# Optimization experiments

Measured on AMD Instinct MI355X. Metric: run time of the kernel, lower is better.

The kernel has to match this reference:

```python
import jax, jax.numpy as jnp
import numpy as np

B, N, K, NUM_CLASSES = 8, 4096, 20, 40


def _knn_idx(x, k):
    # x: [B, N, D] -> indices of k nearest neighbors (self excluded), [B, N, k]
    sq = jnp.sum(x * x, axis=-1)  # [B, N]
    dist = sq[:, :, None] + sq[:, None, :] - 2.0 * jnp.einsum('bnd,bmd->bnm', x, x)
    dist = jnp.where(jnp.eye(x.shape[1], dtype=bool)[None], jnp.inf, dist)
    return jax.lax.top_k(-dist, k)[1]


def _edge_conv(x, idx, params):
    # PyG EdgeConv with max aggregation: max_j MLP([x_i, x_j - x_i])
    x_j = jax.vmap(lambda xb, ib: xb[ib])(x, idx)              # [B, N, K, D]
    x_i = jnp.broadcast_to(x[:, :, None, :], x_j.shape)        # [B, N, K, D]
    h = jnp.concatenate([x_i, x_j - x_i], axis=-1)             # [B, N, K, 2D]
    for w, b in params:
        h = jax.nn.relu(h @ w + b)
    return jnp.max(h, axis=2)                                  # [B, N, out]


def setup_inputs() -> dict:
    key = jax.random.key(0)
    ks = jax.random.split(key, 12)

    def lin(k, i, o):  # torch Linear default init
        k1, k2 = jax.random.split(k)
        s = 1.0 / np.sqrt(i)
        return (jax.random.uniform(k1, (i, o), jnp.float32, -s, s),
                jax.random.uniform(k2, (o,), jnp.float32, -s, s))

    inp = {
        'pos': jax.random.normal(ks[0], (B * N, 3), jnp.float32),
        'batch': jnp.repeat(jnp.arange(B, dtype=jnp.int32), N),
    }
    names = [('m1w1', 'm1b1', 6, 64), ('m1w2', 'm1b2', 64, 64), ('m1w3', 'm1b3', 64, 64),
             ('m2w1', 'm2b1', 128, 128), ('m2w2', 'm2b2', 128, 128), ('m2w3', 'm2b3', 128, 256),
             ('lin0_w', 'lin0_b', 256, 512), ('lin1_w', 'lin1_b', 512, 256),
             ('lin2_w', 'lin2_b', 256, 256), ('lin3_w', 'lin3_b', 256, NUM_CLASSES)]
    for t, (wn, bn, i, o) in enumerate(names):
        w, b = lin(ks[t + 1], i, o)
        inp[wn] = w
        inp[bn] = b
    return inp


def reference(pos, batch, m1w1, m1b1, m1w2, m1b2, m1w3, m1b3,
              m2w1, m2b1, m2w2, m2b2, m2w3, m2b3,
              lin0_w, lin0_b, lin1_w, lin1_b, lin2_w, lin2_b, lin3_w, lin3_b):
    x = pos.reshape(B, N, 3)
    x = _edge_conv(x, _knn_idx(x, K), [(m1w1, m1b1), (m1w2, m1b2), (m1w3, m1b3)])   # [B,N,64]
    x = _edge_conv(x, _knn_idx(x, K), [(m2w1, m2b1), (m2w2, m2b2), (m2w3, m2b3)])   # [B,N,256]
    x = jax.nn.relu(x @ lin0_w + lin0_b)                                            # [B,N,512]
    x = jax.ops.segment_max(x.reshape(B * N, -1), batch, num_segments=B)            # [B,512]
    x = jax.nn.relu(x @ lin1_w + lin1_b)
    x = jax.nn.relu(x @ lin2_w + lin2_b)   # dropout is identity in eval mode
    x = x @ lin3_w + lin3_b
    return jax.nn.log_softmax(x, axis=-1)
```

## Files before the change

### kernel.cpp

```cpp
#include <hip/hip_runtime.h>

#define DEVI static __device__ __forceinline__

typedef __attribute__((ext_vector_type(4))) float f32x4;
typedef __attribute__((ext_vector_type(8))) short short8;
typedef __attribute__((ext_vector_type(4))) short short4v;
typedef __attribute__((ext_vector_type(8))) __bf16 bf16x8;

#define N_    4096
#define KNN_  20
#define NPTS  32768

DEVI unsigned short f2bf(float f){
  unsigned u = __float_as_uint(f);
  u += 0x7FFFu + ((u >> 16) & 1u);
  return (unsigned short)(u >> 16);
}
DEVI float bf2f(unsigned short s){ return __uint_as_float(((unsigned)s) << 16); }
DEVI float bf2fs(short s){ return __uint_as_float(((unsigned)(unsigned short)s) << 16); }
DEVI unsigned umin32(unsigned a, unsigned b){ return a < b ? a : b; }
DEVI unsigned umax32(unsigned a, unsigned b){ return a > b ? a : b; }

DEVI f32x4 mfma16(short8 a, short8 b, f32x4 c){
  return __builtin_amdgcn_mfma_f32_16x16x32_bf16(
      __builtin_bit_cast(bf16x8, a), __builtin_bit_cast(bf16x8, b), c, 0, 0, 0);
}

DEVI short8 lds_frag(const unsigned short* buf, int row, int k0, int strideS, int swzMask){
  return *(const short8*)(buf + row*strideS + (k0 ^ ((row & swzMask) << 3)));
}
DEVI void lds_put8(unsigned short* buf, int row, int k0, int strideS, int swzMask, short8 v){
  *(short8*)(buf + row*strideS + (k0 ^ ((row & swzMask) << 3))) = v;
}
DEVI void lds_put1(unsigned short* buf, int row, int col, int strideS, int swzMask, unsigned short v){
  buf[row*strideS + (col ^ ((row & swzMask) << 3))] = v;
}

DEVI void ins32(unsigned K, unsigned (&a)[20]){
#pragma unroll
  for (int t = 19; t >= 1; --t) a[t] = umin32(a[t], umax32(a[t-1], K));
  a[0] = umin32(a[0], K);
}
DEVI void ins64(double K, double (&a)[20]){
#pragma unroll
  for (int t = 19; t >= 1; --t) a[t] = fmin(a[t], fmax(a[t-1], K));
  a[0] = fmin(a[0], K);
}

__global__ __launch_bounds__(256) void p3_k(const float* __restrict__ pos,
    unsigned short* __restrict__ p3h, unsigned short* __restrict__ p3l, float* __restrict__ nrm3){
  int p = blockIdx.x*256 + threadIdx.x;
  if (p >= NPTS) return;
  float x = pos[(size_t)p*3], y = pos[(size_t)p*3+1], z = pos[(size_t)p*3+2];
  float v[8] = {x, y, z, 0.f, 0.f, 0.f, 0.f, 0.f};
#pragma unroll
  for (int c = 0; c < 8; ++c){
    unsigned short h = f2bf(v[c]);
    p3h[(size_t)p*8 + c] = h;
    p3l[(size_t)p*8 + c] = f2bf(v[c] - bf2f(h));
  }
  nrm3[p] = fmaf(x, x, fmaf(y, y, z*z));
}

template<int MODE>
__global__ __launch_bounds__(256) void knn_k(const unsigned short* __restrict__ Xh,
                                             const unsigned short* __restrict__ Xl,
                                             const float* __restrict__ nrm,
                                             unsigned* __restrict__ pk){
  constexpr int OBL  = MODE ? 8192  : 1024;
  constexpr int OBUF = MODE ? 16384 : 2048;
  constexpr int OTHR = OBUF + 6144;
  constexpr int OSQ  = OTHR + 256;
  constexpr int SM   = MODE ? (OSQ + 256) : 15488;
  __shared__ __align__(16) char smem[SM];
  unsigned short* Bh = (unsigned short*)(smem);
  unsigned short* Bl = (unsigned short*)(smem + OBL);
  unsigned* buf      = (unsigned*)(smem + OBUF);
  unsigned* rowThr   = (unsigned*)(smem + OTHR);
  float* sqj         = (float*)(smem + OSQ);
  unsigned* mD       = (unsigned*)(smem);

  const int blk = blockIdx.x;
  const int rt = blk & 63, ch = (blk >> 6) & 1, bb = blk >> 7;
  const int rowbase = rt * 64, cbase = ch * 2048;
  const size_t gb = (size_t)bb * N_;
  const int tid = threadIdx.x, lane = tid & 63, wid = tid >> 6;
  const int l15 = lane & 15, g = lane >> 4, kL = g << 3, r0 = g << 2;
  const int qidx = wid*16 + l15;

  if (tid < 64) rowThr[tid] = 0xFFFFFFFFu;

  short8 qh0 = {0,0,0,0,0,0,0,0}, qh1 = {0,0,0,0,0,0,0,0};
  short8 ql0 = {0,0,0,0,0,0,0,0}, ql1 = {0,0,0,0,0,0,0,0};
  if (MODE == 1){
    const size_t ab = (gb + rowbase + qidx) * 64;
    qh0 = *(const short8*)(Xh + ab + kL);
    qh1 = *(const short8*)(Xh + ab + 32 + kL);
    ql0 = *(const short8*)(Xl + ab + kL);
    ql1 = *(const short8*)(Xl + ab + 32 + kL);
  } else {
    if (g == 0){
      const size_t ab = (gb + rowbase + qidx) * 8;
      qh0 = *(const short8*)(Xh + ab);
      ql0 = *(const short8*)(Xl + ab);
    }
  }
  const float si = nrm[gb + rowbase + qidx];

  unsigned arr[20];
#pragma unroll
  for (int t = 0; t < 20; ++t) arr[t] = 0xFFFFFFFFu;
  int cnt = 0;
  bool selfR[4];
#pragma unroll
  for (int r = 0; r < 4; ++r) selfR[r] = (l15 == r0 + r);

  if (MODE == 1){
    for (int f = tid; f < 512; f += 256){
      int lf = f & 63, half = (f >> 6) & 1, ct = f >> 7;
      int row = ct*16 + (lf & 15);
      int col = half*32 + ((lf >> 4) << 3);
      const size_t src = (gb + cbase + row) * 64 + col;
      *(short8*)(Bh + f*8) = *(const short8*)(Xh + src);
      *(short8*)(Bl + f*8) = *(const short8*)(Xl + src);
    }
  } else {
    if (tid < 64)       *(short8*)(Bh + tid*8)      = *(const short8*)(Xh + (gb + cbase + tid)*8);
    else if (tid < 128) *(short8*)(Bl + (tid-64)*8) = *(const short8*)(Xl + (gb + cbase + (tid-64))*8);
  }
  if (tid < 64) sqj[tid] = nrm[gb + cbase + tid];
  __syncthreads();

  for (int c = 0; c < 32; ++c){
    const bool selfTile = (cbase + c*64 == rowbase);
    unsigned kb16[16];
#pragma unroll
    for (int ct = 0; ct < 4; ++ct){
      f32x4 acc = {0.f,0.f,0.f,0.f};
      if (MODE == 1){
        const int fb = lane*8;
        short8 ch0 = *(const short8*)(Bh + (ct*2+0)*512 + fb);
        short8 ch1 = *(const short8*)(Bh + (ct*2+1)*512 + fb);
        short8 cl0 = *(const short8*)(Bl + (ct*2+0)*512 + fb);
        short8 cl1 = *(const short8*)(Bl + (ct*2+1)*512 + fb);
        acc = mfma16(ch0, qh0, acc); acc = mfma16(ch1, qh1, acc);
        acc = mfma16(cl0, qh0, acc); acc = mfma16(cl1, qh1, acc);
        acc = mfma16(ch0, ql0, acc); acc = mfma16(ch1, ql1, acc);
      } else {
        short8 cb = {0,0,0,0,0,0,0,0}, cl_ = {0,0,0,0,0,0,0,0};
        if (g == 0){
          cb  = *(const short8*)(Bh + (ct*16 + l15)*8);
          cl_ = *(const short8*)(Bl + (ct*16 + l15)*8);
        }
        acc = mfma16(cb,  qh0, acc);
        acc = mfma16(cl_, qh0, acc);
        acc = mfma16(cb,  ql0, acc);
      }
      f32x4 sj4 = *(const f32x4*)(sqj + ct*16 + r0);
#pragma unroll
      for (int r = 0; r < 4; ++r){
        unsigned cid = (unsigned)(c*64 + ct*16 + r0 + r);
        float dv = fmaxf(fmaf(-2.f, acc[r], si + sj4[r]), 0.f);
        unsigned kb = (__float_as_uint(dv) & ~0x7FFu) | cid;
        if (selfTile && ct == wid && selfR[r]) kb = 0x7F800000u | cid;
        kb16[ct*4 + r] = kb;
      }
    }
    short8 nh0 = {0,0,0,0,0,0,0,0}, nh1 = {0,0,0,0,0,0,0,0};
    short8 nl0 = {0,0,0,0,0,0,0,0}, nl1 = {0,0,0,0,0,0,0,0};
    float nsq = 0.f;
    const bool more = (c + 1 < 32);
    if (more){
      if (MODE == 1){
#pragma unroll
        for (int ff = 0; ff < 2; ++ff){
          int f = tid + ff*256;
          int lf = f & 63, half = (f >> 6) & 1, ct = f >> 7;
          int row = ct*16 + (lf & 15);
          int col = half*32 + ((lf >> 4) << 3);
          const size_t src = (gb + cbase + (c+1)*64 + row) * 64 + col;
          if (ff == 0){ nh0 = *(const short8*)(Xh + src); nl0 = *(const short8*)(Xl + src); }
          else        { nh1 = *(const short8*)(Xh + src); nl1 = *(const short8*)(Xl + src); }
        }
      } else {
        if (tid < 64)       nh0 = *(const short8*)(Xh + (gb + cbase + (c+1)*64 + tid)*8);
        else if (tid < 128) nl0 = *(const short8*)(Xl + (gb + cbase + (c+1)*64 + (tid-64))*8);
      }
      if (tid < 64) nsq = nrm[gb + cbase + (c+1)*64 + tid];
    }
    {
      unsigned thrP = rowThr[qidx];
#pragma unroll
      for (int i = 0; i < 16; ++i){
        unsigned kb = kb16[i];
        if (kb < thrP){
          if (cnt < 6){ buf[cnt*256 + tid] = kb; ++cnt; }
          else ins32(kb, arr);
        }
      }
      for (int t = 0; t < cnt; ++t) ins32(buf[t*256 + tid], arr);
      cnt = 0;
      atomicMin(&rowThr[qidx], arr[19]);
    }
    __syncthreads();
    if (more){
      if (MODE == 1){
        *(short8*)(Bh + tid*8)       = nh0;
        *(short8*)(Bh + (tid+256)*8) = nh1;
        *(short8*)(Bl + tid*8)       = nl0;
        *(short8*)(Bl + (tid+256)*8) = nl1;
      } else {
        if (tid < 64)       *(short8*)(Bh + tid*8)      = nh0;
        else if (tid < 128) *(short8*)(Bl + (tid-64)*8) = nl0;
      }
      if (tid < 64) sqj[tid] = nsq;
    }
    __syncthreads();
  }
  __syncthreads();
  if (g > 0){
#pragma unroll
    for (int t = 0; t < 20; ++t) mD[(qidx*3 + g-1)*20 + t] = arr[t];
  }
  __syncthreads();
  if (g == 0){
    for (int gg = 0; gg < 3; ++gg)
#pragma unroll
      for (int t = 0; t < 20; ++t) ins32(mD[(qidx*3 + gg)*20 + t], arr);
    const size_t gp = gb + rowbase + qidx;
#pragma unroll
    for (int t = 0; t < 20; ++t) pk[((size_t)(ch*20 + t))*NPTS + gp] = arr[t];
  }
}

__global__ __launch_bounds__(256) void knn_merge_k(const unsigned* __restrict__ pk,
                                                   int* __restrict__ idx){
  const int p = blockIdx.x*256 + threadIdx.x;
  double arr[20];
#pragma unroll
  for (int t = 0; t < 20; ++t){
    unsigned k = pk[(size_t)t*NPTS + p];
    unsigned long long K = (((unsigned long long)(k & ~0x7FFu)) << 1) | (k & 0x7FFu);
    arr[t] = __builtin_bit_cast(double, K);
  }
#pragma unroll
  for (int t = 0; t < 20; ++t){
    unsigned k = pk[(size_t)(20 + t)*NPTS + p];
    unsigned long long K = (((unsigned long long)(k & ~0x7FFu)) << 1) | (2048u + (k & 0x7FFu));
    ins64(__builtin_bit_cast(double, K), arr);
  }
  int* o = idx + (size_t)p*KNN_;
#pragma unroll
  for (int t = 0; t < 20; ++t)
    o[t] = (int)(__builtin_bit_cast(unsigned long long, arr[t]) & 0xFFFu);
}

__global__ void stage_w_k(const float* __restrict__ src, unsigned short* __restrict__ dh,
                          unsigned short* __restrict__ dl, int K, int Nw, int KT, int NT){
  int tid = blockIdx.x*256 + threadIdx.x;
  if (tid >= NT*KT*64) return;
  int l = tid & 63;
  int kk = (tid >> 6) % KT;
  int nt = tid / (64*KT);
  int n = nt*16 + (l & 15);
  int kb = kk*32 + ((l >> 4) << 3);
#pragma unroll
  for (int e=0;e<8;++e){
    int k = kb + e;
    float w = (k < K) ? src[(size_t)k*Nw + n] : 0.f;
    unsigned short h = f2bf(w);
    dh[(size_t)tid*8 + e] = h;
    if (dl) dl[(size_t)tid*8 + e] = f2bf(w - bf2f(h));
  }
}

__global__ __launch_bounds__(256) void ec1_k(const float* __restrict__ pos, const int* __restrict__ idx1,
    const unsigned short* __restrict__ W1h, const unsigned short* __restrict__ W1l,
    const unsigned short* __restrict__ W2h, const unsigned short* __restrict__ W2l,
    const unsigned short* __restrict__ W3h, const unsigned short* __restrict__ W3l,
    const float* __restrict__ b1, const float* __restrict__ b2, const float* __restrict__ b3,
    unsigned short* __restrict__ x1h, unsigned short* __restrict__ x1l, float* __restrict__ nrm1){
  __shared__ __align__(16) char smem[52224];
  unsigned short* Ah  = (unsigned short*)(smem);
  unsigned short* Al  = (unsigned short*)(smem + 5120);
  unsigned short* H1h = (unsigned short*)(smem + 10240);
  unsigned short* H1l = (unsigned short*)(smem + 20480);
  unsigned short* H2h = (unsigned short*)(smem + 30720);
  unsigned short* H2l = (unsigned short*)(smem + 40960);
  unsigned* pmax = (unsigned*)(smem + 51200);
  const int p0 = blockIdx.x * 4;
  const int bb = p0 >> 12;
  const int tid = threadIdx.x, lane = tid & 63, wid = tid >> 6;
  pmax[tid] = 0u;
  if (tid < 80){
    int p = p0 + tid/20, slot = tid%20;
    int j = idx1[(size_t)p*KNN_ + slot];
    int gj = (bb << 12) + j;
    float a6[6];
    a6[0] = pos[(size_t)p*3]; a6[1] = pos[(size_t)p*3+1]; a6[2] = pos[(size_t)p*3+2];
    a6[3] = pos[(size_t)gj*3]   - a6[0];
    a6[4] = pos[(size_t)gj*3+1] - a6[1];
    a6[5] = pos[(size_t)gj*3+2] - a6[2];
#pragma unroll
    for (int q=0;q<4;++q){
      short8 vh, vl;
#pragma unroll
      for (int c=0;c<8;++c){
        int cc = q*8+c;
        float v = 0.f;
        if (cc < 6) v = a6[cc];
        unsigned short h = f2bf(v);
        vh[c] = (short)h;
        vl[c] = (short)f2bf(v - bf2f(h));
      }
      lds_put8(Ah, tid, q*8, 32, 3, vh);
      lds_put8(Al, tid, q*8, 32, 3, vl);
    }
  }
  __syncthreads();
  const int l15 = lane & 15, kL = (lane >> 4) << 3, r0 = (lane >> 4) << 2;
  {
    int nt = wid;
    short8 wh = *(const short8*)(W1h + ((size_t)nt*64 + lane)*8);
    short8 wl = *(const short8*)(W1l + ((size_t)nt*64 + lane)*8);
    float bias = b1[nt*16 + l15];
    for (int mt=0; mt<5; ++mt){
      int ar = mt*16 + l15;
      short8 ah = lds_frag(Ah, ar, kL, 32, 3);
      short8 al = lds_frag(Al, ar, kL, 32, 3);
      f32x4 acc = {0.f,0.f,0.f,0.f};
      acc = mfma16(ah, wh, acc);
      acc = mfma16(ah, wl, acc);
      acc = mfma16(al, wh, acc);
#pragma unroll
      for (int r=0;r<4;++r){
        int row = mt*16 + r0 + r;
        float v = fmaxf(acc[r] + bias, 0.f);
        unsigned short h = f2bf(v);
        lds_put1(H1h, row, nt*16+l15, 64, 7, h);
        lds_put1(H1l, row, nt*16+l15, 64, 7, f2bf(v - bf2f(h)));
      }
    }
  }
  __syncthreads();
  {
    int nt = wid;
    short8 wh0 = *(const short8*)(W2h + ((size_t)(nt*2+0)*64 + lane)*8);
    short8 wh1 = *(const short8*)(W2h + ((size_t)(nt*2+1)*64 + lane)*8);
    short8 wl0 = *(const short8*)(W2l + ((size_t)(nt*2+0)*64 + lane)*8);
    short8 wl1 = *(const short8*)(W2l + ((size_t)(nt*2+1)*64 + lane)*8);
    float bias = b2[nt*16 + l15];
    for (int mt=0; mt<5; ++mt){
      int ar = mt*16 + l15;
      short8 ah0 = lds_frag(H1h, ar, kL,      64, 7);
      short8 ah1 = lds_frag(H1h, ar, 32 + kL, 64, 7);
      short8 al0 = lds_frag(H1l, ar, kL,      64, 7);
      short8 al1 = lds_frag(H1l, ar, 32 + kL, 64, 7);
      f32x4 acc = {0.f,0.f,0.f,0.f};
      acc = mfma16(ah0, wh0, acc); acc = mfma16(ah1, wh1, acc);
      acc = mfma16(ah0, wl0, acc); acc = mfma16(ah1, wl1, acc);
      acc = mfma16(al0, wh0, acc); acc = mfma16(al1, wh1, acc);
#pragma unroll
      for (int r=0;r<4;++r){
        int row = mt*16 + r0 + r;
        float v = fmaxf(acc[r] + bias, 0.f);
        unsigned short h = f2bf(v);
        lds_put1(H2h, row, nt*16+l15, 64, 7, h);
        lds_put1(H2l, row, nt*16+l15, 64, 7, f2bf(v - bf2f(h)));
      }
    }
  }
  __syncthreads();
  {
    int nt = wid;
    short8 wh0 = *(const short8*)(W3h + ((size_t)(nt*2+0)*64 + lane)*8);
    short8 wh1 = *(const short8*)(W3h + ((size_t)(nt*2+1)*64 + lane)*8);
    short8 wl0 = *(const short8*)(W3l + ((size_t)(nt*2+0)*64 + lane)*8);
    short8 wl1 = *(const short8*)(W3l + ((size_t)(nt*2+1)*64 + lane)*8);
    float bias = b3[nt*16 + l15];
    for (int mt=0; mt<5; ++mt){
      int ar = mt*16 + l15;
      short8 ah0 = lds_frag(H2h, ar, kL,      64, 7);
      short8 ah1 = lds_frag(H2h, ar, 32 + kL, 64, 7);
      short8 al0 = lds_frag(H2l, ar, kL,      64, 7);
      short8 al1 = lds_frag(H2l, ar, 32 + kL, 64, 7);
      f32x4 acc = {0.f,0.f,0.f,0.f};
      acc = mfma16(ah0, wh0, acc); acc = mfma16(ah1, wh1, acc);
      acc = mfma16(ah0, wl0, acc); acc = mfma16(ah1, wl1, acc);
      acc = mfma16(al0, wh0, acc); acc = mfma16(al1, wh1, acc);
#pragma unroll
      for (int r=0;r<4;++r){
        int row = mt*16 + r0 + r;
        float v = fmaxf(acc[r] + bias, 0.f);
        atomicMax(&pmax[(row/20)*64 + nt*16 + l15], __float_as_uint(v));
      }
    }
  }
  __syncthreads();
  if (tid < 128){
    int p = tid >> 5, cp = tid & 31;
    int c0 = cp*2, c1 = c0 + 1;
    float m0 = __uint_as_float(pmax[p*64 + c0]);
    float m1 = __uint_as_float(pmax[p*64 + c1]);
    int gp = p0 + p;
    unsigned short h0 = f2bf(m0), h1v = f2bf(m1);
    x1h[(size_t)gp*64 + c0] = h0;
    x1h[(size_t)gp*64 + c1] = h1v;
    x1l[(size_t)gp*64 + c0] = f2bf(m0 - bf2f(h0));
    x1l[(size_t)gp*64 + c1] = f2bf(m1 - bf2f(h1v));
    float s = fmaf(m0, m0, m1*m1);
    s += __shfl_xor(s, 1, 32); s += __shfl_xor(s, 2, 32); s += __shfl_xor(s, 4, 32);
    s += __shfl_xor(s, 8, 32); s += __shfl_xor(s, 16, 32);
    if (cp == 0) nrm1[gp] = s;
  }
}

__global__ __launch_bounds__(256) void ec2_k(const unsigned short* __restrict__ x1h, const int* __restrict__ idx2,
    const unsigned short* __restrict__ V1, const unsigned short* __restrict__ V2, const unsigned short* __restrict__ V3,
    const float* __restrict__ b1, const float* __restrict__ b2, const float* __restrict__ b3,
    unsigned short* __restrict__ x2b){
  __shared__ __align__(16) char smem[81920];
  unsigned short* A  = (unsigned short*)(smem);
  unsigned short* H1 = (unsigned short*)(smem + 40960);
  const int p0 = blockIdx.x * 8, bb = p0 >> 12;
  const int tid = threadIdx.x, lane = tid & 63, wid = tid >> 6;
  const int l15 = lane & 15, r0 = (lane >> 4) << 2;

  if (tid < 160){
    int p = p0 + tid/20, slot = tid%20;
    int j = idx2[(size_t)p*KNN_ + slot];
    int gj = (bb << 12) + j;
    const unsigned short* xi = x1h + (size_t)p*64;
    const unsigned short* xj = x1h + (size_t)gj*64;
    int mt = tid >> 4, lrow = tid & 15;
#pragma unroll
    for (int q=0;q<8;++q){
      short8 vi = *(const short8*)(xi + q*8);
      short8 vj = *(const short8*)(xj + q*8);
      short8 vd;
#pragma unroll
      for (int c=0;c<8;++c) vd[c] = (short)f2bf(bf2fs(vj[c]) - bf2fs(vi[c]));
      *(short8*)(A + (((mt*4 + (q>>2))*64) + (q&3)*16 + lrow)*8) = vi;
      *(short8*)(A + (((mt*4 + 2 + (q>>2))*64) + (q&3)*16 + lrow)*8) = vd;
    }
  }
  __syncthreads();

  {
    short8 w[2][4];
#pragma unroll
    for (int ni=0;ni<2;++ni)
#pragma unroll
      for (int kk=0;kk<4;++kk)
        w[ni][kk] = *(const short8*)(V1 + ((size_t)((wid*2+ni)*4+kk)*64 + lane)*8);
    f32x4 b4[2];
    b4[0] = *(const f32x4*)(b1 + (wid*2+0)*16 + r0);
    b4[1] = *(const f32x4*)(b1 + (wid*2+1)*16 + r0);
    for (int mt=0; mt<10; ++mt){
      short8 bfr[4];
#pragma unroll
      for (int kk=0;kk<4;++kk) bfr[kk] = *(const short8*)(A + ((mt*4+kk)*64 + lane)*8);
#pragma unroll
      for (int ni=0;ni<2;++ni){
        int nt = wid*2 + ni;
        f32x4 acc = {0.f,0.f,0.f,0.f};
#pragma unroll
        for (int kk=0;kk<4;++kk) acc = mfma16(w[ni][kk], bfr[kk], acc);
        short4v v4;
#pragma unroll
        for (int r=0;r<4;++r) v4[r] = (short)f2bf(fmaxf(acc[r] + b4[ni][r], 0.f));
        int kk2 = nt >> 1, sub2 = (nt & 1)*2 + (r0 >> 3);
        *(short4v*)(H1 + ((mt*4+kk2)*64 + sub2*16 + l15)*8 + (r0 & 4)) = v4;
      }
    }
  }
  __syncthreads();
  {
    short8 w[2][4];
#pragma unroll
    for (int ni=0;ni<2;++ni)
#pragma unroll
      for (int kk=0;kk<4;++kk)
        w[ni][kk] = *(const short8*)(V2 + ((size_t)((wid*2+ni)*4+kk)*64 + lane)*8);
    f32x4 b4[2];
    b4[0] = *(const f32x4*)(b2 + (wid*2+0)*16 + r0);
    b4[1] = *(const f32x4*)(b2 + (wid*2+1)*16 + r0);
    for (int mt=0; mt<10; ++mt){
      short8 bfr[4];
#pragma unroll
      for (int kk=0;kk<4;++kk) bfr[kk] = *(const short8*)(H1 + ((mt*4+kk)*64 + lane)*8);
#pragma unroll
      for (int ni=0;ni<2;++ni){
        int nt = wid*2 + ni;
        f32x4 acc = {0.f,0.f,0.f,0.f};
#pragma unroll
        for (int kk=0;kk<4;++kk) acc = mfma16(w[ni][kk], bfr[kk], acc);
        short4v v4;
#pragma unroll
        for (int r=0;r<4;++r) v4[r] = (short)f2bf(fmaxf(acc[r] + b4[ni][r], 0.f));
        int kk2 = nt >> 1, sub2 = (nt & 1)*2 + (r0 >> 3);
        *(short4v*)(A + ((mt*4+kk2)*64 + sub2*16 + l15)*8 + (r0 & 4)) = v4;
      }
    }
  }
  __syncthreads();
  for (int g2=0; g2<2; ++g2){
    {
      short8 w[2][4];
#pragma unroll
      for (int ni=0;ni<2;++ni)
#pragma unroll
        for (int kk=0;kk<4;++kk)
          w[ni][kk] = *(const short8*)(V3 + ((size_t)((g2*8 + wid*2+ni)*4+kk)*64 + lane)*8);
      f32x4 b4[2];
      b4[0] = *(const f32x4*)(b3 + (g2*8 + wid*2+0)*16 + r0);
      b4[1] = *(const f32x4*)(b3 + (g2*8 + wid*2+1)*16 + r0);
      for (int mt=0; mt<10; ++mt){
        short8 bfr[4];
#pragma unroll
        for (int kk=0;kk<4;++kk) bfr[kk] = *(const short8*)(A + ((mt*4+kk)*64 + lane)*8);
#pragma unroll
        for (int ni=0;ni<2;++ni){
          int ntl = wid*2 + ni;
          f32x4 acc = {0.f,0.f,0.f,0.f};
#pragma unroll
          for (int kk=0;kk<4;++kk) acc = mfma16(w[ni][kk], bfr[kk], acc);
          short4v v4;
#pragma unroll
          for (int r=0;r<4;++r) v4[r] = (short)f2bf(fmaxf(acc[r] + b4[ni][r], 0.f));
          int kk2 = ntl >> 1, sub2 = (ntl & 1)*2 + (r0 >> 3);
          *(short4v*)(H1 + ((mt*4+kk2)*64 + sub2*16 + l15)*8 + (r0 & 4)) = v4;
        }
      }
    }
    __syncthreads();
    if (tid < 128){
      int p = tid >> 4, c8 = tid & 15;
      int kk = c8 >> 2, sub = c8 & 3;
      unsigned short mx[8];
#pragma unroll
      for (int e=0;e<8;++e) mx[e] = 0;
      for (int e=0;e<20;++e){
        int ee = e + p + c8; ee -= (ee >= 20) ? 20 : 0; ee -= (ee >= 20) ? 20 : 0;
        int row = p*20 + ee;
        short8 v = *(const short8*)(H1 + (((row>>4)*4 + kk)*64 + sub*16 + (row & 15))*8);
#pragma unroll
        for (int k2=0;k2<8;++k2){
          unsigned short u = (unsigned short)v[k2];
          mx[k2] = u > mx[k2] ? u : mx[k2];
        }
      }
      short8 o;
#pragma unroll
      for (int k2=0;k2<8;++k2) o[k2] = (short)mx[k2];
      *(short8*)(x2b + (size_t)(p0 + p)*256 + g2*128 + c8*8) = o;
    }
    __syncthreads();
  }
}

__global__ __launch_bounds__(256) void lin0_k(const unsigned short* __restrict__ x2b, const unsigned short* __restrict__ W0s,
                                              const float* __restrict__ b0, unsigned* __restrict__ pool){
  __shared__ __align__(16) char smem[67584];
  unsigned short* A = (unsigned short*)(smem);
  unsigned* ploc = (unsigned*)(smem + 65536);
  const int blk = blockIdx.x; const size_t row0 = (size_t)blk * 128; const int bb = blk >> 5;
  const int tid = threadIdx.x, lane = tid & 63, wid = tid >> 6;
  for (int it = tid; it < 4096; it += 256){
    int row = it >> 5, q = (it & 31) << 3;
    lds_put8(A, row, q, 256, 7, *(const short8*)(x2b + (row0 + row)*256 + q));
  }
  ploc[tid] = 0u; ploc[tid+256] = 0u;
  __syncthreads();
  const int l15 = lane & 15, kL = (lane >> 4) << 3;
  short8 af[2][8];
#pragma unroll
  for (int m=0;m<2;++m)
#pragma unroll
    for (int kk=0;kk<8;++kk)
      af[m][kk] = lds_frag(A, (wid*2+m)*16 + l15, kk*32 + kL, 256, 7);
  for (int nt=0; nt<32; ++nt){
    f32x4 a0 = {0.f,0.f,0.f,0.f}, a1 = {0.f,0.f,0.f,0.f};
#pragma unroll
    for (int kk=0;kk<8;++kk){
      short8 w = *(const short8*)(W0s + ((size_t)(nt*8+kk)*64 + lane)*8);
      a0 = mfma16(af[0][kk], w, a0);
      a1 = mfma16(af[1][kk], w, a1);
    }
    int col = nt*16 + l15;
    float m = fmaxf(fmaxf(fmaxf(a0[0],a0[1]),fmaxf(a0[2],a0[3])),
                    fmaxf(fmaxf(a1[0],a1[1]),fmaxf(a1[2],a1[3])));
    m = fmaxf(m + b0[col], 0.f);
    atomicMax(&ploc[col], __float_as_uint(m));
  }
  __syncthreads();
  atomicMax(&pool[(size_t)bb*512 + tid], ploc[tid]);
  atomicMax(&pool[(size_t)bb*512 + tid + 256], ploc[tid+256]);
}

__global__ __launch_bounds__(256) void head_k(const unsigned* __restrict__ pool,
    const float* __restrict__ w1, const float* __restrict__ bb1,
    const float* __restrict__ w2, const float* __restrict__ bb2,
    const float* __restrict__ w3, const float* __restrict__ bb3,
    float* __restrict__ out){
  __shared__ float pl[8*512];
  __shared__ float y1[8*256];
  __shared__ float y2[8*256];
  __shared__ float lg[8*40];
  const int tid = threadIdx.x;
  for (int it = tid; it < 4096; it += 256) pl[it] = __uint_as_float(pool[it]);
  __syncthreads();
  {
    float acc[8]; float bv = bb1[tid];
#pragma unroll
    for (int r=0;r<8;++r) acc[r] = bv;
    for (int k=0;k<512;++k){
      float w = w1[(size_t)k*256 + tid];
#pragma unroll
      for (int r=0;r<8;++r) acc[r] = fmaf(pl[r*512+k], w, acc[r]);
    }
#pragma unroll
    for (int r=0;r<8;++r) y1[r*256+tid] = fmaxf(acc[r], 0.f);
  }
  __syncthreads();
  {
    float acc[8]; float bv = bb2[tid];
#pragma unroll
    for (int r=0;r<8;++r) acc[r] = bv;
    for (int k=0;k<256;++k){
      float w = w2[(size_t)k*256 + tid];
#pragma unroll
      for (int r=0;r<8;++r) acc[r] = fmaf(y1[r*256+k], w, acc[r]);
    }
#pragma unroll
    for (int r=0;r<8;++r) y2[r*256+tid] = fmaxf(acc[r], 0.f);
  }
  __syncthreads();
  if (tid < 40){
    float acc[8]; float bv = bb3[tid];
#pragma unroll
    for (int r=0;r<8;++r) acc[r] = bv;
    for (int k=0;k<256;++k){
      float w = w3[(size_t)k*40 + tid];
#pragma unroll
      for (int r=0;r<8;++r) acc[r] = fmaf(y2[r*256+k], w, acc[r]);
    }
#pragma unroll
    for (int r=0;r<8;++r) lg[r*40+tid] = acc[r];
  }
  __syncthreads();
  if (tid < 8){
    float m = -__builtin_inff();
    for (int c2=0;c2<40;++c2) m = fmaxf(m, lg[tid*40+c2]);
    float s = 0.f;
    for (int c2=0;c2<40;++c2) s += expf(lg[tid*40+c2] - m);
    float L = logf(s);
    for (int c2=0;c2<40;++c2) out[tid*40+c2] = lg[tid*40+c2] - m - L;
  }
}

extern "C" void kernel_launch(void* const* d_in, const int* in_sizes, int n_in,
                              void* d_out, int out_size, void* d_ws, size_t ws_size,
                              hipStream_t stream){
  (void)in_sizes; (void)n_in; (void)out_size; (void)ws_size;
  const float* pos  = (const float*)d_in[0];
  const float* m1w1 = (const float*)d_in[2];  const float* m1b1 = (const float*)d_in[3];
  const float* m1w2 = (const float*)d_in[4];  const float* m1b2 = (const float*)d_in[5];
  const float* m1w3 = (const float*)d_in[6];  const float* m1b3 = (const float*)d_in[7];
  const float* m2w1 = (const float*)d_in[8];  const float* m2b1 = (const float*)d_in[9];
  const float* m2w2 = (const float*)d_in[10]; const float* m2b2 = (const float*)d_in[11];
  const float* m2w3 = (const float*)d_in[12]; const float* m2b3 = (const float*)d_in[13];
  const float* l0w  = (const float*)d_in[14]; const float* l0b  = (const float*)d_in[15];
  const float* l1w  = (const float*)d_in[16]; const float* l1b  = (const float*)d_in[17];
  const float* l2w  = (const float*)d_in[18]; const float* l2b  = (const float*)d_in[19];
  const float* l3w  = (const float*)d_in[20]; const float* l3b  = (const float*)d_in[21];

  char* ws = (char*)d_ws;
  size_t o = 0;
  auto alloc = [&](size_t bytes){ size_t r = o; o += (bytes + 255) & ~(size_t)255; return r; };
  size_t o_idx1 = alloc((size_t)NPTS*20*4);
  size_t o_idx2 = alloc((size_t)NPTS*20*4);
  size_t o_x1h  = alloc((size_t)NPTS*64*2);
  size_t o_x1l  = alloc((size_t)NPTS*64*2);
  size_t o_nrm  = alloc((size_t)NPTS*4);
  size_t o_x2b  = alloc((size_t)NPTS*256*2);
  size_t o_pool = alloc(8*512*4);
  size_t o_p3h  = alloc((size_t)NPTS*8*2);
  size_t o_p3l  = alloc((size_t)NPTS*8*2);
  size_t o_nrm3 = alloc((size_t)NPTS*4);
  size_t o_pk   = alloc((size_t)2*20*NPTS*4);
  size_t o_W1h = alloc(4*1*64*8*2),  o_W1l = alloc(4*1*64*8*2);
  size_t o_W2h = alloc(4*2*64*8*2),  o_W2l = alloc(4*2*64*8*2);
  size_t o_W3h = alloc(4*2*64*8*2),  o_W3l = alloc(4*2*64*8*2);
  size_t o_V1  = alloc(8*4*64*8*2);
  size_t o_V2  = alloc(8*4*64*8*2);
  size_t o_V3  = alloc(16*4*64*8*2);
  size_t o_W0  = alloc(32*8*64*8*2);

  hipMemsetAsync(ws + o_pool, 0, 8*512*4, stream);

  stage_w_k<<<1,256,0,stream>>>(m1w1, (unsigned short*)(ws+o_W1h), (unsigned short*)(ws+o_W1l), 6, 64, 1, 4);
  stage_w_k<<<2,256,0,stream>>>(m1w2, (unsigned short*)(ws+o_W2h), (unsigned short*)(ws+o_W2l), 64, 64, 2, 4);
  stage_w_k<<<2,256,0,stream>>>(m1w3, (unsigned short*)(ws+o_W3h), (unsigned short*)(ws+o_W3l), 64, 64, 2, 4);
  stage_w_k<<<8,256,0,stream>>>(m2w1, (unsigned short*)(ws+o_V1), nullptr, 128, 128, 4, 8);
  stage_w_k<<<8,256,0,stream>>>(m2w2, (unsigned short*)(ws+o_V2), nullptr, 128, 128, 4, 8);
  stage_w_k<<<16,256,0,stream>>>(m2w3, (unsigned short*)(ws+o_V3), nullptr, 128, 256, 4, 16);
  stage_w_k<<<64,256,0,stream>>>(l0w,  (unsigned short*)(ws+o_W0), nullptr, 256, 512, 8, 32);

  p3_k<<<128,256,0,stream>>>(pos, (unsigned short*)(ws+o_p3h), (unsigned short*)(ws+o_p3l), (float*)(ws+o_nrm3));

  knn_k<0><<<1024,256,0,stream>>>((const unsigned short*)(ws+o_p3h), (const unsigned short*)(ws+o_p3l),
                                  (const float*)(ws+o_nrm3), (unsigned*)(ws+o_pk));
  knn_merge_k<<<128,256,0,stream>>>((const unsigned*)(ws+o_pk), (int*)(ws+o_idx1));

  ec1_k<<<8192,256,0,stream>>>(pos, (const int*)(ws+o_idx1),
      (const unsigned short*)(ws+o_W1h), (const unsigned short*)(ws+o_W1l),
      (const unsigned short*)(ws+o_W2h), (const unsigned short*)(ws+o_W2l),
      (const unsigned short*)(ws+o_W3h), (const unsigned short*)(ws+o_W3l),
      m1b1, m1b2, m1b3,
      (unsigned short*)(ws+o_x1h), (unsigned short*)(ws+o_x1l), (float*)(ws+o_nrm));

  knn_k<1><<<1024,256,0,stream>>>((const unsigned short*)(ws+o_x1h), (const unsigned short*)(ws+o_x1l),
                                  (const float*)(ws+o_nrm), (unsigned*)(ws+o_pk));
  knn_merge_k<<<128,256,0,stream>>>((const unsigned*)(ws+o_pk), (int*)(ws+o_idx2));

  ec2_k<<<4096,256,0,stream>>>((const unsigned short*)(ws+o_x1h), (const int*)(ws+o_idx2),
      (const unsigned short*)(ws+o_V1), (const unsigned short*)(ws+o_V2), (const unsigned short*)(ws+o_V3),
      m2b1, m2b2, m2b3, (unsigned short*)(ws+o_x2b));

  lin0_k<<<256,256,0,stream>>>((const unsigned short*)(ws+o_x2b), (const unsigned short*)(ws+o_W0),
                               l0b, (unsigned*)(ws+o_pool));

  head_k<<<1,256,0,stream>>>((const unsigned*)(ws+o_pool), l1w, l1b, l2w, l2b, l3w, l3b, (float*)d_out);
}
```

Baseline: 656.1 us.

## Double-buffer kNN column tiles and restructure EdgeConv1 MLP LDS layout

The kNN kernel now keeps two LDS buffers for the candidate column tile. The next tile's global loads are issued before the MFMA and top-k work, which removes one barrier per iteration and hides load latency. The first EdgeConv kernel swaps the MFMA operand order so each lane writes four contiguous outputs straight into fragment-ordered LDS, replacing scattered scalar swizzled stores. It also replaces the per-element LDS atomicMax with a dump-then-reduce pass. The cost is doubled LDS use in kNN, which may lower occupancy, plus an extra reduction pass in EdgeConv.

```diff
diff --git a/kernel.cpp b/kernel.cpp
--- a/kernel.cpp
+++ b/kernel.cpp
@@ -31,9 +31,6 @@
 }
 DEVI void lds_put8(unsigned short* buf, int row, int k0, int strideS, int swzMask, short8 v){
   *(short8*)(buf + row*strideS + (k0 ^ ((row & swzMask) << 3))) = v;
-}
-DEVI void lds_put1(unsigned short* buf, int row, int col, int strideS, int swzMask, unsigned short v){
-  buf[row*strideS + (col ^ ((row & swzMask) << 3))] = v;
 }
 
 DEVI void ins32(unsigned K, unsigned (&a)[20]){
@@ -67,17 +64,18 @@
                                              const unsigned short* __restrict__ Xl,
                                              const float* __restrict__ nrm,
                                              unsigned* __restrict__ pk){
-  constexpr int OBL  = MODE ? 8192  : 1024;
-  constexpr int OBUF = MODE ? 16384 : 2048;
+  constexpr int BSTR = MODE ? 4096 : 512;
+  constexpr int OBL  = MODE ? 16384 : 2048;
+  constexpr int OBUF = MODE ? 32768 : 4096;
   constexpr int OTHR = OBUF + 6144;
   constexpr int OSQ  = OTHR + 256;
-  constexpr int SM   = MODE ? (OSQ + 256) : 15488;
+  constexpr int SM   = MODE ? (OSQ + 512) : 15360;
   __shared__ __align__(16) char smem[SM];
-  unsigned short* Bh = (unsigned short*)(smem);
-  unsigned short* Bl = (unsigned short*)(smem + OBL);
+  unsigned short* BhA = (unsigned short*)(smem);
+  unsigned short* BlA = (unsigned short*)(smem + OBL);
   unsigned* buf      = (unsigned*)(smem + OBUF);
   unsigned* rowThr   = (unsigned*)(smem + OTHR);
-  float* sqj         = (float*)(smem + OSQ);
+  float* sqjA        = (float*)(smem + OSQ);
   unsigned* mD       = (unsigned*)(smem);
 
   const int blk = blockIdx.x;
@@ -121,18 +119,46 @@
       int row = ct*16 + (lf & 15);
       int col = half*32 + ((lf >> 4) << 3);
       const size_t src = (gb + cbase + row) * 64 + col;
-      *(short8*)(Bh + f*8) = *(const short8*)(Xh + src);
-      *(short8*)(Bl + f*8) = *(const short8*)(Xl + src);
+      *(short8*)(BhA + f*8) = *(const short8*)(Xh + src);
+      *(short8*)(BlA + f*8) = *(const short8*)(Xl + src);
     }
   } else {
-    if (tid < 64)       *(short8*)(Bh + tid*8)      = *(const short8*)(Xh + (gb + cbase + tid)*8);
-    else if (tid < 128) *(short8*)(Bl + (tid-64)*8) = *(const short8*)(Xl + (gb + cbase + (tid-64))*8);
-  }
-  if (tid < 64) sqj[tid] = nrm[gb + cbase + tid];
+    if (tid < 64)       *(short8*)(BhA + tid*8)      = *(const short8*)(Xh + (gb + cbase + tid)*8);
+    else if (tid < 128) *(short8*)(BlA + (tid-64)*8) = *(const short8*)(Xl + (gb + cbase + (tid-64))*8);
+  }
+  if (tid < 64) sqjA[tid] = nrm[gb + cbase + tid];
   __syncthreads();
 
   for (int c = 0; c < 32; ++c){
+    const int cur = c & 1;
+    const unsigned short* Bh = BhA + cur*BSTR;
+    const unsigned short* Bl = BlA + cur*BSTR;
+    const float* sqj = sqjA + cur*64;
     const bool selfTile = (cbase + c*64 == rowbase);
+    const bool more = (c + 1 < 32);
+
+    short8 nh0 = {0,0,0,0,0,0,0,0}, nh1 = {0,0,0,0,0,0,0,0};
+    short8 nl0 = {0,0,0,0,0,0,0,0}, nl1 = {0,0,0,0,0,0,0,0};
+    float nsq = 0.f;
+    if (more){
+      if (MODE == 1){
+#pragma unroll
+        for (int ff = 0; ff < 2; ++ff){
+          int f = tid + ff*256;
+          int lf = f & 63, half = (f >> 6) & 1, ct = f >> 7;
+          int row = ct*16 + (lf & 15);
+          int col = half*32 + ((lf >> 4) << 3);
+          const size_t src = (gb + cbase + (c+1)*64 + row) * 64 + col;
+          if (ff == 0){ nh0 = *(const short8*)(Xh + src); nl0 = *(const short8*)(Xl + src); }
+          else        { nh1 = *(const short8*)(Xh + src); nl1 = *(const short8*)(Xl + src); }
+        }
+      } else {
+        if (tid < 64)       nh0 = *(const short8*)(Xh + (gb + cbase + (c+1)*64 + tid)*8);
+        else if (tid < 128) nl0 = *(const short8*)(Xl + (gb + cbase + (c+1)*64 + (tid-64))*8);
+      }
+      if (tid < 64) nsq = nrm[gb + cbase + (c+1)*64 + tid];
+    }
+
     unsigned kb16[16];
 #pragma unroll
     for (int ct = 0; ct < 4; ++ct){
@@ -166,28 +192,7 @@
         kb16[ct*4 + r] = kb;
       }
     }
-    short8 nh0 = {0,0,0,0,0,0,0,0}, nh1 = {0,0,0,0,0,0,0,0};
-    short8 nl0 = {0,0,0,0,0,0,0,0}, nl1 = {0,0,0,0,0,0,0,0};
-    float nsq = 0.f;
-    const bool more = (c + 1 < 32);
-    if (more){
-      if (MODE == 1){
-#pragma unroll
-        for (int ff = 0; ff < 2; ++ff){
-          int f = tid + ff*256;
-          int lf = f & 63, half = (f >> 6) & 1, ct = f >> 7;
-          int row = ct*16 + (lf & 15);
-          int col = half*32 + ((lf >> 4) << 3);
-          const size_t src = (gb + cbase + (c+1)*64 + row) * 64 + col;
-          if (ff == 0){ nh0 = *(const short8*)(Xh + src); nl0 = *(const short8*)(Xl + src); }
-          else        { nh1 = *(const short8*)(Xh + src); nl1 = *(const short8*)(Xl + src); }
-        }
-      } else {
-        if (tid < 64)       nh0 = *(const short8*)(Xh + (gb + cbase + (c+1)*64 + tid)*8);
-        else if (tid < 128) nl0 = *(const short8*)(Xl + (gb + cbase + (c+1)*64 + (tid-64))*8);
-      }
-      if (tid < 64) nsq = nrm[gb + cbase + (c+1)*64 + tid];
-    }
+
     {
       unsigned thrP = rowThr[qidx];
 #pragma unroll
@@ -202,18 +207,20 @@
       cnt = 0;
       atomicMin(&rowThr[qidx], arr[19]);
     }
-    __syncthreads();
+
     if (more){
+      unsigned short* BhN = BhA + (cur^1)*BSTR;
+      unsigned short* BlN = BlA + (cur^1)*BSTR;
       if (MODE == 1){
-        *(short8*)(Bh + tid*8)       = nh0;
-        *(short8*)(Bh + (tid+256)*8) = nh1;
-        *(short8*)(Bl + tid*8)       = nl0;
-        *(short8*)(Bl + (tid+256)*8) = nl1;
+        *(short8*)(BhN + tid*8)       = nh0;
+        *(short8*)(BhN + (tid+256)*8) = nh1;
+        *(short8*)(BlN + tid*8)       = nl0;
+        *(short8*)(BlN + (tid+256)*8) = nl1;
       } else {
-        if (tid < 64)       *(short8*)(Bh + tid*8)      = nh0;
-        else if (tid < 128) *(short8*)(Bl + (tid-64)*8) = nl0;
-      }
-      if (tid < 64) sqj[tid] = nsq;
+        if (tid < 64)       *(short8*)(BhN + tid*8)      = nh0;
+        else if (tid < 128) *(short8*)(BlN + (tid-64)*8) = nl0;
+      }
+      if (tid < 64) sqjA[(cur^1)*64 + tid] = nsq;
     }
     __syncthreads();
   }
@@ -280,18 +287,19 @@
     const unsigned short* __restrict__ W3h, const unsigned short* __restrict__ W3l,
     const float* __restrict__ b1, const float* __restrict__ b2, const float* __restrict__ b3,
     unsigned short* __restrict__ x1h, unsigned short* __restrict__ x1l, float* __restrict__ nrm1){
-  __shared__ __align__(16) char smem[52224];
+  __shared__ __align__(16) char smem[51200];
   unsigned short* Ah  = (unsigned short*)(smem);
   unsigned short* Al  = (unsigned short*)(smem + 5120);
   unsigned short* H1h = (unsigned short*)(smem + 10240);
   unsigned short* H1l = (unsigned short*)(smem + 20480);
   unsigned short* H2h = (unsigned short*)(smem + 30720);
   unsigned short* H2l = (unsigned short*)(smem + 40960);
-  unsigned* pmax = (unsigned*)(smem + 51200);
+  float* dump = (float*)(smem);
   const int p0 = blockIdx.x * 4;
   const int bb = p0 >> 12;
   const int tid = threadIdx.x, lane = tid & 63, wid = tid >> 6;
-  pmax[tid] = 0u;
+  const int l15 = lane & 15, g = lane >> 4, r0 = g << 2;
+
   if (tid < 80){
     int p = p0 + tid/20, slot = tid%20;
     int j = idx1[(size_t)p*KNN_ + slot];
@@ -301,117 +309,126 @@
     a6[3] = pos[(size_t)gj*3]   - a6[0];
     a6[4] = pos[(size_t)gj*3+1] - a6[1];
     a6[5] = pos[(size_t)gj*3+2] - a6[2];
-#pragma unroll
-    for (int q=0;q<4;++q){
-      short8 vh, vl;
-#pragma unroll
-      for (int c=0;c<8;++c){
-        int cc = q*8+c;
-        float v = 0.f;
-        if (cc < 6) v = a6[cc];
-        unsigned short h = f2bf(v);
-        vh[c] = (short)h;
-        vl[c] = (short)f2bf(v - bf2f(h));
-      }
-      lds_put8(Ah, tid, q*8, 32, 3, vh);
-      lds_put8(Al, tid, q*8, 32, 3, vl);
-    }
-  }
-  __syncthreads();
-  const int l15 = lane & 15, kL = (lane >> 4) << 3, r0 = (lane >> 4) << 2;
+    int mt = tid >> 4, lrow = tid & 15;
+    short8 vh, vl, zz = {0,0,0,0,0,0,0,0};
+#pragma unroll
+    for (int c=0;c<8;++c){
+      float v = (c < 6) ? a6[c] : 0.f;
+      unsigned short h = f2bf(v);
+      vh[c] = (short)h;
+      vl[c] = (short)f2bf(v - bf2f(h));
+    }
+    *(short8*)(Ah + (mt*64 + lrow)*8) = vh;
+    *(short8*)(Al + (mt*64 + lrow)*8) = vl;
+#pragma unroll
+    for (int gg=1;gg<4;++gg){
+      *(short8*)(Ah + (mt*64 + gg*16 + lrow)*8) = zz;
+      *(short8*)(Al + (mt*64 + gg*16 + lrow)*8) = zz;
+    }
+  }
+  __syncthreads();
+  const int nt = wid;
+  const int kk2 = nt >> 1, sub2 = (nt & 1)*2 + (g >> 1), e0 = (g & 1)*4;
   {
-    int nt = wid;
     short8 wh = *(const short8*)(W1h + ((size_t)nt*64 + lane)*8);
     short8 wl = *(const short8*)(W1l + ((size_t)nt*64 + lane)*8);
-    float bias = b1[nt*16 + l15];
+    f32x4 b4 = *(const f32x4*)(b1 + nt*16 + r0);
     for (int mt=0; mt<5; ++mt){
-      int ar = mt*16 + l15;
-      short8 ah = lds_frag(Ah, ar, kL, 32, 3);
-      short8 al = lds_frag(Al, ar, kL, 32, 3);
+      short8 ah = *(const short8*)(Ah + (mt*64 + lane)*8);
+      short8 al = *(const short8*)(Al + (mt*64 + lane)*8);
       f32x4 acc = {0.f,0.f,0.f,0.f};
-      acc = mfma16(ah, wh, acc);
-      acc = mfma16(ah, wl, acc);
-      acc = mfma16(al, wh, acc);
+      acc = mfma16(wh, ah, acc);
+      acc = mfma16(wl, ah, acc);
+      acc = mfma16(wh, al, acc);
+      short4v vh4, vl4;
 #pragma unroll
       for (int r=0;r<4;++r){
-        int row = mt*16 + r0 + r;
-        float v = fmaxf(acc[r] + bias, 0.f);
+        float v = fmaxf(acc[r] + b4[r], 0.f);
         unsigned short h = f2bf(v);
-        lds_put1(H1h, row, nt*16+l15, 64, 7, h);
-        lds_put1(H1l, row, nt*16+l15, 64, 7, f2bf(v - bf2f(h)));
-      }
+        vh4[r] = (short)h;
+        vl4[r] = (short)f2bf(v - bf2f(h));
+      }
+      *(short4v*)(H1h + ((mt*2 + kk2)*64 + sub2*16 + l15)*8 + e0) = vh4;
+      *(short4v*)(H1l + ((mt*2 + kk2)*64 + sub2*16 + l15)*8 + e0) = vl4;
     }
   }
   __syncthreads();
   {
-    int nt = wid;
     short8 wh0 = *(const short8*)(W2h + ((size_t)(nt*2+0)*64 + lane)*8);
     short8 wh1 = *(const short8*)(W2h + ((size_t)(nt*2+1)*64 + lane)*8);
     short8 wl0 = *(const short8*)(W2l + ((size_t)(nt*2+0)*64 + lane)*8);
     short8 wl1 = *(const short8*)(W2l + ((size_t)(nt*2+1)*64 + lane)*8);
-    float bias = b2[nt*16 + l15];
+    f32x4 b4 = *(const f32x4*)(b2 + nt*16 + r0);
     for (int mt=0; mt<5; ++mt){
-      int ar = mt*16 + l15;
-      short8 ah0 = lds_frag(H1h, ar, kL,      64, 7);
-      short8 ah1 = lds_frag(H1h, ar, 32 + kL, 64, 7);
-      short8 al0 = lds_frag(H1l, ar, kL,      64, 7);
-      short8 al1 = lds_frag(H1l, ar, 32 + kL, 64, 7);
+      short8 ah0 = *(const short8*)(H1h + ((mt*2+0)*64 + lane)*8);
+      short8 ah1 = *(const short8*)(H1h + ((mt*2+1)*64 + lane)*8);
+      short8 al0 = *(const short8*)(H1l + ((mt*2+0)*64 + lane)*8);
+      short8 al1 = *(const short8*)(H1l + ((mt*2+1)*64 + lane)*8);
       f32x4 acc = {0.f,0.f,0.f,0.f};
-      acc = mfma16(ah0, wh0, acc); acc = mfma16(ah1, wh1, acc);
-      acc = mfma16(ah0, wl0, acc); acc = mfma16(ah1, wl1, acc);
-      acc = mfma16(al0, wh0, acc); acc = mfma16(al1, wh1, acc);
+      acc = mfma16(wh0, ah0, acc); acc = mfma16(wh1, ah1, acc);
+      acc = mfma16(wl0, ah0, acc); acc = mfma16(wl1, ah1, acc);
+      acc = mfma16(wh0, al0, acc); acc = mfma16(wh1, al1, acc);
+      short4v vh4, vl4;
 #pragma unroll
       for (int r=0;r<4;++r){
-        int row = mt*16 + r0 + r;
-        float v = fmaxf(acc[r] + bias, 0.f);
+        float v = fmaxf(acc[r] + b4[r], 0.f);
         unsigned short h = f2bf(v);
-        lds_put1(H2h, row, nt*16+l15, 64, 7, h);
-        lds_put1(H2l, row, nt*16+l15, 64, 7, f2bf(v - bf2f(h)));
-      }
+        vh4[r] = (short)h;
+        vl4[r] = (short)f2bf(v - bf2f(h));
+      }
+      *(short4v*)(H2h + ((mt*2 + kk2)*64 + sub2*16 + l15)*8 + e0) = vh4;
+      *(short4v*)(H2l + ((mt*2 + kk2)*64 + sub2*16 + l15)*8 + e0) = vl4;
     }
   }
   __syncthreads();
   {
-    int nt = wid;
     short8 wh0 = *(const short8*)(W3h + ((size_t)(nt*2+0)*64 + lane)*8);
     short8 wh1 = *(const short8*)(W3h + ((size_t)(nt*2+1)*64 + lane)*8);
     short8 wl0 = *(const short8*)(W3l + ((size_t)(nt*2+0)*64 + lane)*8);
     short8 wl1 = *(const short8*)(W3l + ((size_t)(nt*2+1)*64 + lane)*8);
-    float bias = b3[nt*16 + l15];
+    f32x4 b4 = *(const f32x4*)(b3 + nt*16 + r0);
     for (int mt=0; mt<5; ++mt){
-      int ar = mt*16 + l15;
-      short8 ah0 = lds_frag(H2h, ar, kL,      64, 7);
-      short8 ah1 = lds_frag(H2h, ar, 32 + kL, 64, 7);
-      short8 al0 = lds_frag(H2l, ar, kL,      64, 7);
-      short8 al1 = lds_frag(H2l, ar, 32 + kL, 64, 7);
+      short8 ah0 = *(const short8*)(H2h + ((mt*2+0)*64 + lane)*8);
+      short8 ah1 = *(const short8*)(H2h + ((mt*2+1)*64 + lane)*8);
+      short8 al0 = *(const short8*)(H2l + ((mt*2+0)*64 + lane)*8);
+      short8 al1 = *(const short8*)(H2l + ((mt*2+1)*64 + lane)*8);
       f32x4 acc = {0.f,0.f,0.f,0.f};
-      acc = mfma16(ah0, wh0, acc); acc = mfma16(ah1, wh1, acc);
-      acc = mfma16(ah0, wl0, acc); acc = mfma16(ah1, wl1, acc);
-      acc = mfma16(al0, wh0, acc); acc = mfma16(al1, wh1, acc);
-#pragma unroll
-      for (int r=0;r<4;++r){
-        int row = mt*16 + r0 + r;
-        float v = fmaxf(acc[r] + bias, 0.f);
-        atomicMax(&pmax[(row/20)*64 + nt*16 + l15], __float_as_uint(v));
-      }
-    }
-  }
-  __syncthreads();
-  if (tid < 128){
-    int p = tid >> 5, cp = tid & 31;
-    int c0 = cp*2, c1 = c0 + 1;
-    float m0 = __uint_as_float(pmax[p*64 + c0]);
-    float m1 = __uint_as_float(pmax[p*64 + c1]);
+      acc = mfma16(wh0, ah0, acc); acc = mfma16(wh1, ah1, acc);
+      acc = mfma16(wl0, ah0, acc); acc = mfma16(wl1, ah1, acc);
+      acc = mfma16(wh0, al0, acc); acc = mfma16(wh1, al1, acc);
+      f32x4 o;
+#pragma unroll
+      for (int r=0;r<4;++r) o[r] = fmaxf(acc[r] + b4[r], 0.f);
+      int edge = mt*16 + l15;
+      *(f32x4*)(dump + edge*68 + nt*16 + r0) = o;
+    }
+  }
+  __syncthreads();
+  if (tid < 64){
+    int p = tid >> 4, c4 = tid & 15;
+    int st = tid % 20;
+    float mx[4] = {0.f,0.f,0.f,0.f};
+    for (int e=0;e<20;++e){
+      int ee = st + e; if (ee >= 20) ee -= 20;
+      f32x4 v = *(const f32x4*)(dump + (p*20 + ee)*68 + c4*4);
+#pragma unroll
+      for (int r=0;r<4;++r) mx[r] = fmaxf(mx[r], v[r]);
+    }
     int gp = p0 + p;
-    unsigned short h0 = f2bf(m0), h1v = f2bf(m1);
-    x1h[(size_t)gp*64 + c0] = h0;
-    x1h[(size_t)gp*64 + c1] = h1v;
-    x1l[(size_t)gp*64 + c0] = f2bf(m0 - bf2f(h0));
-    x1l[(size_t)gp*64 + c1] = f2bf(m1 - bf2f(h1v));
-    float s = fmaf(m0, m0, m1*m1);
-    s += __shfl_xor(s, 1, 32); s += __shfl_xor(s, 2, 32); s += __shfl_xor(s, 4, 32);
-    s += __shfl_xor(s, 8, 32); s += __shfl_xor(s, 16, 32);
-    if (cp == 0) nrm1[gp] = s;
+    short4v h4, l4;
+    float s = 0.f;
+#pragma unroll
+    for (int r=0;r<4;++r){
+      float m = mx[r];
+      unsigned short h = f2bf(m);
+      h4[r] = (short)h;
+      l4[r] = (short)f2bf(m - bf2f(h));
+      s = fmaf(m, m, s);
+    }
+    *(short4v*)(x1h + (size_t)gp*64 + c4*4) = h4;
+    *(short4v*)(x1l + (size_t)gp*64 + c4*4) = l4;
+    s += __shfl_xor(s, 1); s += __shfl_xor(s, 2); s += __shfl_xor(s, 4); s += __shfl_xor(s, 8);
+    if (c4 == 0) nrm1[gp] = s;
   }
 }
 
```

New measurement: 656.3 us. About the same (+0.0%).
